# Optimization experiments

Hardware: AMD Instinct MI355X
Metric: run time of the kernel (lower is better)

Reference implementation:

```python
import jax, jax.numpy as jnp
import numpy as np

B, C, H, W = 1, 256, 512, 512
DS = 4
HD, WD = H // DS, W // DS
N_NOISE = 32
N_CLUSTERS = 8


def setup_inputs() -> dict:
    key = jax.random.key(0)
    k1, k2, k3, k4, k5 = jax.random.split(key, 5)
    x = jax.random.normal(k1, (B, C, H, W), dtype=jnp.float32)
    # deterministic 'HDBSCAN' labels over the B*C=256 channel-tokens:
    # first 224 channels in 8 clusters of 28, last 32 channels are noise (-1)
    n_clustered = C - N_NOISE
    labels_np = np.concatenate([
        np.arange(n_clustered) % N_CLUSTERS,
        -np.ones(N_NOISE, dtype=np.int64),
    ]).astype(np.int32)
    labels = jnp.asarray(labels_np)
    noise_idx = jnp.arange(n_clustered, C, dtype=jnp.int32)  # channels with label -1
    # grouped 1x1 conv (groups=C, 3 outputs per channel): per-output scalar weight+bias
    w_qkv = jax.random.normal(k2, (3 * C,), dtype=jnp.float32) * 0.02
    b_qkv = jax.random.normal(k3, (3 * C,), dtype=jnp.float32) * 0.02
    # depthwise ConvTranspose2d(kernel=stride=DS, groups=C): per-channel DSxDS kernel
    w_up = jax.random.normal(k4, (C, DS, DS), dtype=jnp.float32) * 0.25
    b_up = jax.random.normal(k5, (C,), dtype=jnp.float32) * 0.02
    return {"x": x, "labels": labels, "noise_idx": noise_idx,
            "w_qkv": w_qkv, "b_qkv": b_qkv, "w_up": w_up, "b_up": b_up}


def _l2norm(a):
    n = jnp.linalg.norm(a, axis=-1, keepdims=True)
    return a / jnp.maximum(n, 1e-12)


def reference(x, labels, noise_idx, w_qkv, b_qkv, w_up, b_up):
    # --- MaxPool2d(DS, DS) ---  (B=1)
    xd = x.reshape(C, HD, DS, WD, DS).max(axis=(2, 4))          # (C, HD, WD)
    xdf = xd.reshape(C, HD * WD)                                 # (C, hw)
    # --- grouped 1x1 qkv conv: out channel o = x[o//3]*w[o]+b[o]; then chunk(3)
    #     reproduces the torch code exactly, incl. its interleaved channel layout ---
    qkv = jnp.repeat(xdf, 3, axis=0) * w_qkv[:, None] + b_qkv[:, None]  # (3C, hw)
    q, k, v = qkv[:C], qkv[C:2 * C], qkv[2 * C:]
    # --- per-cluster attention as a single masked softmax over C tokens ---
    valid = labels != -1
    same = (labels[:, None] == labels[None, :]) & valid[:, None] & valid[None, :]
    scores = q @ k.T                                             # (C, C), no scaling (as in source)
    scores = jnp.where(same, scores, jnp.finfo(scores.dtype).min)
    attn = jax.nn.softmax(scores, axis=-1)
    attn = jnp.where(valid[:, None], attn, 0.0)                  # noise rows -> 0 output
    out_ds = attn @ v                                            # (C, hw)
    # --- depthwise ConvTranspose2d, stride==kernel -> non-overlapping blocks ---
    out_sp = out_ds.reshape(C, HD, WD)
    up = jnp.einsum('chw,cab->chawb', out_sp, w_up).reshape(C, H, W)
    up = (up + b_up[:, None, None])[None]                        # (1, C, H, W)
    # --- noise features & cosine similarity ---
    nf = x.reshape(B, C, H * W)[:, noise_idx, :]                 # (B, n_noise, HW)
    cf = up.reshape(B, C, H * W)                                 # (B, C, HW)
    sim = jnp.einsum('bch,bnh->bcn', _l2norm(cf), _l2norm(nf)).mean(axis=-1)  # (B, C)
    similar = sim.reshape(B, C, 1, 1)
    out = up + (1.0 - similar) * x
    return out, nf.reshape(B, N_NOISE, H, W)
```

## Files before the change

### kernel.cpp

```cpp
#include <hip/hip_runtime.h>
#include <math.h>

#define C_ 256
#define H_ 512
#define W_ 512
#define HW_ (H_*W_)
#define HD_ 128
#define WD_ 128
#define P_ (HD_*WD_)
#define NN_ 32
#define GR_ 86
#define NSL_ 128

#define XD_OFF     0ull
#define SDS_OFF    4194304ull
#define GT_OFF     8388608ull
#define GPART_OFF  8650752ull
#define DSTP_OFF   8650752ull
#define S_OFF      9641984ull
#define SPART_OFF  9642240ull
#define NSQP_OFF   9650432ull
#define GSUMP_OFF  9651456ull
#define BETA_OFF   9651968ull
#define M_OFF      9652224ull
#define SCALE_OFF  9674752ull

typedef float nfloat4 __attribute__((ext_vector_type(4)));

__device__ __forceinline__ void nt_store4(float4 v, float* p) {
    nfloat4 nv;
    nv.x = v.x; nv.y = v.y; nv.z = v.z; nv.w = v.w;
    __builtin_nontemporal_store(nv, (nfloat4*)p);
}

__device__ __forceinline__ float4 nt_load4(const float* p) {
    nfloat4 nv = __builtin_nontemporal_load((const nfloat4*)p);
    float4 v;
    v.x = nv.x; v.y = nv.y; v.z = nv.z; v.w = nv.w;
    return v;
}

__device__ __forceinline__ float wsum64(float v) {
#pragma unroll
    for (int off = 32; off > 0; off >>= 1) v += __shfl_down(v, off, 64);
    return v;
}

__global__ void __launch_bounds__(256) k_pre(
        const float* __restrict__ x, const int* __restrict__ nidx,
        float* __restrict__ xd, float* __restrict__ outnf,
        float* __restrict__ Spart, float* __restrict__ nsqp) {
    int b = blockIdx.x;
    int c = b >> 5, seg = b & 31;
    int t = threadIdx.x;
    __shared__ int sn;
    if (t == 0) {
        int nn = -1;
        for (int n = 0; n < NN_; n++)
            if (nidx[n] == c) nn = n;
        sn = nn;
    }
    __syncthreads();
    int n = sn;
    int wd = t & 127;
    int hl = t >> 7;
    float ssum = 0.f, ss = 0.f;
    const float* xc = x + (size_t)c * HW_;
    float* nfc = outnf + (size_t)(n < 0 ? 0 : n) * HW_;
#pragma unroll
    for (int q = 0; q < 2; q++) {
        int hd = 4 * seg + hl + 2 * q;
        const float4* xr = (const float4*)(xc + (size_t)(4 * hd) * W_) + wd;
        float4 r0 = xr[0], r1 = xr[128], r2 = xr[256], r3 = xr[384];
        if (n >= 0) {
            float* nr = nfc + (size_t)(4 * hd) * W_ + 4 * wd;
            nt_store4(r0, nr);
            nt_store4(r1, nr + 512);
            nt_store4(r2, nr + 1024);
            nt_store4(r3, nr + 1536);
            ss += r0.x*r0.x + r0.y*r0.y + r0.z*r0.z + r0.w*r0.w
                + r1.x*r1.x + r1.y*r1.y + r1.z*r1.z + r1.w*r1.w
                + r2.x*r2.x + r2.y*r2.y + r2.z*r2.z + r2.w*r2.w
                + r3.x*r3.x + r3.y*r3.y + r3.z*r3.z + r3.w*r3.w;
        }
        float m0 = fmaxf(fmaxf(r0.x, r0.y), fmaxf(r0.z, r0.w));
        float m1 = fmaxf(fmaxf(r1.x, r1.y), fmaxf(r1.z, r1.w));
        float m2 = fmaxf(fmaxf(r2.x, r2.y), fmaxf(r2.z, r2.w));
        float m3 = fmaxf(fmaxf(r3.x, r3.y), fmaxf(r3.z, r3.w));
        float m = fmaxf(fmaxf(m0, m1), fmaxf(m2, m3));
        xd[(size_t)c * P_ + (size_t)hd * WD_ + wd] = m;
        ssum += m;
    }
    __shared__ float red[4];
    float tt = wsum64(ssum);
    int wid = t >> 6, ln = t & 63;
    if (ln == 0) red[wid] = tt;
    __syncthreads();
    if (t == 0) Spart[c * 32 + seg] = red[0] + red[1] + red[2] + red[3];
    if (n >= 0) {
        __syncthreads();
        float t2 = wsum64(ss);
        if (ln == 0) red[wid] = t2;
        __syncthreads();
        if (t == 0) nsqp[n * 32 + seg] = red[0] + red[1] + red[2] + red[3];
    }
}

__global__ void __launch_bounds__(256) k_mid(
        const float* __restrict__ x, const int* __restrict__ nidx,
        const float* __restrict__ nsqp, const float* __restrict__ Spart,
        const float* __restrict__ xd,
        float* __restrict__ gt, float* __restrict__ gsump,
        float* __restrict__ gpart, float* __restrict__ S) {
    __shared__ float smem[2 * 32 * 132];
    int bid = blockIdx.x;
    int t = threadIdx.x;
    if (bid < 512) {
        float* inv_ = smem;
        int* ncs = (int*)(smem + 32);
        float* red = smem + 64;
        float4* comb = (float4*)(smem + 128);
        if (t < NN_) {
            const float* np = nsqp + t * 32;
            float s = 0.f;
#pragma unroll
            for (int k = 0; k < 32; k++) s += np[k];
            inv_[t] = (1.f / 32.f) / fmaxf(sqrtf(s), 1e-12f);
            ncs[t] = nidx[t];
        }
        __syncthreads();
        int h = bid >> 2, a = bid & 3;
        int w = t & 127, half = t >> 7;
        size_t rowoff = (size_t)(4 * h + a) * W_ + 4 * w;
        float4 acc = make_float4(0.f, 0.f, 0.f, 0.f);
#pragma unroll
        for (int k = 0; k < 16; k++) {
            int n = half * 16 + k;
            float4 v = *(const float4*)(x + (size_t)ncs[n] * HW_ + rowoff);
            float iv = inv_[n];
            acc.x += v.x * iv; acc.y += v.y * iv;
            acc.z += v.z * iv; acc.w += v.w * iv;
        }
        comb[t] = acc;
        float gs = acc.x + acc.y + acc.z + acc.w;
        float tt = wsum64(gs);
        int wid = t >> 6, ln = t & 63;
        if (ln == 0) red[wid] = tt;
        __syncthreads();
        if (t == 0) gsump[bid] = red[0] + red[1] + red[2] + red[3];
        if (t < 128) {
            float4 u = comb[t], v2 = comb[t + 128];
            float g0 = u.x + v2.x, g1 = u.y + v2.y, g2 = u.z + v2.z, g3 = u.w + v2.w;
            size_t pbase = (size_t)(a * 4) * P_ + h * WD_ + w;
            gt[pbase] = g0;
            gt[pbase + P_] = g1;
            gt[pbase + 2 * P_] = g2;
            gt[pbase + 3 * P_] = g3;
        }
    } else if (bid < 512 + NSL_) {
        int sl = bid - 512;
        float (*As)[132] = (float(*)[132])smem;
        float (*Bs)[132] = (float(*)[132])(smem + 32 * 132);
        int tx = t & 15, ty = t >> 4;
        int p0 = sl * 128;
        float acc[8][8];
#pragma unroll
        for (int i = 0; i < 8; i++)
#pragma unroll
            for (int j = 0; j < 8; j++) acc[i][j] = 0.f;
        for (int ch = 0; ch < 4; ch++) {
            int pb = p0 + ch * 32;
            __syncthreads();
#pragma unroll
            for (int kk = 0; kk < 16; kk++) {
                int lin = kk * 256 + t;
                int row = lin >> 5;
                int pp = lin & 31;
                float av = 0.f, bv = 0.f;
                if (row < GR_) {
                    av = xd[(size_t)row * P_ + pb + pp];
                    bv = xd[(size_t)(85 + row) * P_ + pb + pp];
                }
                As[pp][row] = av;
                Bs[pp][row] = bv;
            }
            __syncthreads();
            for (int pp = 0; pp < 32; pp++) {
                float4 fa0 = *(const float4*)&As[pp][8 * tx];
                float4 fa1 = *(const float4*)&As[pp][8 * tx + 4];
                float4 fb0 = *(const float4*)&Bs[pp][8 * ty];
                float4 fb1 = *(const float4*)&Bs[pp][8 * ty + 4];
                float fa[8] = {fa0.x, fa0.y, fa0.z, fa0.w, fa1.x, fa1.y, fa1.z, fa1.w};
                float fb[8] = {fb0.x, fb0.y, fb0.z, fb0.w, fb1.x, fb1.y, fb1.z, fb1.w};
#pragma unroll
                for (int ii = 0; ii < 8; ii++)
#pragma unroll
                    for (int jj = 0; jj < 8; jj++) acc[ii][jj] += fa[ii] * fb[jj];
            }
        }
        float* gp = gpart + (size_t)sl * 7744;
#pragma unroll
        for (int ii = 0; ii < 8; ii++) {
            int ga = 8 * tx + ii;
            if (ga < GR_) {
#pragma unroll
                for (int jj = 0; jj < 8; jj++) {
                    int gb = 8 * ty + jj;
                    if (gb < GR_) gp[ga * 88 + gb] = acc[ii][jj];
                }
            }
        }
    } else {
        if (t < C_) {
            const float* sp = Spart + t * 32;
            float s = 0.f;
#pragma unroll
            for (int k = 0; k < 32; k++) s += sp[k];
            S[t] = s;
        }
    }
}

__global__ void __launch_bounds__(256) k_attn(
        const int* __restrict__ labels, const float* __restrict__ wqkv,
        const float* __restrict__ bqkv, const float* __restrict__ gpart,
        const float* __restrict__ S, float* __restrict__ M,
        float* __restrict__ beta) {
    int i = blockIdx.x, j = threadIdx.x;
    __shared__ float grow[GR_];
    __shared__ float Mloc[GR_];
    __shared__ float red[4];
    __shared__ float bc;
    int li = labels[i];
    if (li < 0) {
        if (j < GR_) M[i * 88 + j] = 0.f;
        if (j == 0) beta[i] = 0.f;
        return;
    }
    int a = i / 3;
    if (j < GR_) {
        Mloc[j] = 0.f;
        const float* gp = gpart + (size_t)a * 88 + j;
        float s = 0.f;
#pragma unroll 8
        for (int sl = 0; sl < NSL_; sl++) s += gp[(size_t)sl * 7744];
        grow[j] = s;
    }
    __syncthreads();
    float wq = wqkv[i], bq = bqkv[i];
    int kidx = 256 + j;
    int bk = kidx / 3;
    float wk = wqkv[kidx], bkb = bqkv[kidx];
    int lj = labels[j];
    bool same = (lj == li);
    float score = -3.0e38f;
    if (same)
        score = wq * wk * grow[bk - 85] + wq * bkb * S[a] + bq * wk * S[bk] +
                16384.f * bq * bkb;
    int wid = j >> 6, ln = j & 63;
    float m = score;
#pragma unroll
    for (int off = 32; off > 0; off >>= 1) m = fmaxf(m, __shfl_down(m, off, 64));
    if (ln == 0) red[wid] = m;
    __syncthreads();
    if (j == 0) bc = fmaxf(fmaxf(red[0], red[1]), fmaxf(red[2], red[3]));
    __syncthreads();
    float mx = bc;
    float e = same ? expf(score - mx) : 0.f;
    __syncthreads();
    float t = wsum64(e);
    if (ln == 0) red[wid] = t;
    __syncthreads();
    if (j == 0) bc = red[0] + red[1] + red[2] + red[3];
    __syncthreads();
    float attn = e / bc;
    int vidx = 512 + j;
    int vr = vidx / 3 - 170;
    float wv = wqkv[vidx], bv = bqkv[vidx];
    __syncthreads();
    float bp = wsum64(attn * bv);
    if (ln == 0) red[wid] = bp;
    __syncthreads();
    if (j == 0) beta[i] = red[0] + red[1] + red[2] + red[3];
    atomicAdd(&Mloc[vr], attn * wv);
    __syncthreads();
    if (j < GR_) M[i * 88 + j] = Mloc[j];
}

__global__ void __launch_bounds__(256) k_outds(
        const float* __restrict__ xd, const float* __restrict__ gt,
        const float* __restrict__ M, const float* __restrict__ beta,
        float* __restrict__ sds, float* __restrict__ dstp) {
    __shared__ float Mt[16][88];
    __shared__ float bt[16];
    __shared__ float sdsL[16][258];
    __shared__ float gtsL[16][258];
    int t = threadIdx.x;
    int p0 = blockIdx.x * 256;
    int i0 = blockIdx.y * 16;
    for (int idx = t; idx < 16 * 88; idx += 256)
        Mt[idx / 88][idx % 88] = M[(size_t)(i0 + idx / 88) * 88 + (idx % 88)];
    if (t < 16) bt[t] = beta[i0 + t];
#pragma unroll 4
    for (int ab = 0; ab < 16; ab++)
        gtsL[ab][t] = gt[(size_t)ab * P_ + p0 + t];
    __syncthreads();
    float acc[16];
#pragma unroll
    for (int ii = 0; ii < 16; ii++) acc[ii] = bt[ii];
    const float* xb = xd + (size_t)170 * P_ + p0 + t;
    for (int r = 0; r < 84; r += 4) {
        float x0 = xb[(size_t)r * P_];
        float x1 = xb[(size_t)(r + 1) * P_];
        float x2 = xb[(size_t)(r + 2) * P_];
        float x3 = xb[(size_t)(r + 3) * P_];
#pragma unroll
        for (int ii = 0; ii < 16; ii++) {
            float4 mv = *(const float4*)&Mt[ii][r];
            acc[ii] += mv.x * x0 + mv.y * x1 + mv.z * x2 + mv.w * x3;
        }
    }
    {
        float x0 = xb[(size_t)84 * P_];
        float x1 = xb[(size_t)85 * P_];
#pragma unroll
        for (int ii = 0; ii < 16; ii++)
            acc[ii] += Mt[ii][84] * x0 + Mt[ii][85] * x1;
    }
#pragma unroll
    for (int ii = 0; ii < 16; ii++) {
        sds[(size_t)(i0 + ii) * P_ + p0 + t] = acc[ii];
        sdsL[ii][t] = acc[ii];
    }
    __syncthreads();
    int ch = t & 15, ab = t >> 4;
    bool do1 = (t < 16), do2 = (t >= 16 && t < 32);
    float D = 0.f, sx = 0.f;
    for (int k = 0; k < 256; k++) {
        float sv = sdsL[ch][k];
        float gv = gtsL[ab][k];
        D += sv * gv;
        if (do1) sx += sv;
        if (do2) sx += sv * sv;
    }
    size_t base = ((size_t)(i0 + ch) * 64 + blockIdx.x) * 18;
    dstp[base + ab] = D;
    if (do1) dstp[base + 16] = sx;
    if (do2) dstp[base + 17] = sx;
}

__global__ void __launch_bounds__(64) k_sim(
        const float* __restrict__ dstp, const float* __restrict__ gsump,
        const float* __restrict__ wup, const float* __restrict__ bup,
        float* __restrict__ scale) {
    int c = blockIdx.x, t = threadIdx.x;
    const float* dp = dstp + ((size_t)c * 64 + t) * 18;
    float vals[19];
#pragma unroll
    for (int q = 0; q < 18; q++) vals[q] = dp[q];
    float gsl = 0.f;
#pragma unroll
    for (int k = 0; k < 8; k++) gsl += gsump[t + 64 * k];
    vals[18] = gsl;
#pragma unroll
    for (int q = 0; q < 19; q++) vals[q] = wsum64(vals[q]);
    if (t == 0) {
        float gs = vals[18];
        float wsm = 0.f, wsq = 0.f, dd = 0.f;
#pragma unroll
        for (int ab = 0; ab < 16; ab++) {
            float w = wup[c * 16 + ab];
            wsm += w;
            wsq += w * w;
            dd += w * vals[ab];
        }
        float s1 = vals[16], s2 = vals[17];
        float b = bup[c];
        float dot = dd + b * gs;
        float n2 = wsq * s2 + 2.f * b * wsm * s1 + (float)HW_ * b * b;
        float nrm = sqrtf(fmaxf(n2, 0.f));
        scale[c] = 1.f - dot / fmaxf(nrm, 1e-12f);
    }
}

__global__ void __launch_bounds__(256) k_final(
        const float* __restrict__ x, const float* __restrict__ sds,
        const float* __restrict__ wup, const float* __restrict__ bup,
        const float* __restrict__ scale, float* __restrict__ out) {
    int bid = blockIdx.x;
    int c = bid >> 7, hd = bid & 127;
    int t = threadIdx.x;
    int wq = t & 127, ysub = t >> 7;
    float sv = sds[(size_t)c * P_ + (size_t)hd * WD_ + wq];
    float b = bup[c];
    float sc = scale[c];
    float4 wu0 = *(const float4*)(wup + c * 16 + ysub * 4);
    float4 wu1 = *(const float4*)(wup + c * 16 + (ysub + 2) * 4);
    size_t xoff = ((size_t)c * H_ + 4 * hd + ysub) * W_ + 4 * wq;
    float4 x0 = nt_load4(x + xoff);
    float4 x1 = nt_load4(x + xoff + 2 * W_);
    float4 o0, o1;
    o0.x = sv * wu0.x + b + sc * x0.x;
    o0.y = sv * wu0.y + b + sc * x0.y;
    o0.z = sv * wu0.z + b + sc * x0.z;
    o0.w = sv * wu0.w + b + sc * x0.w;
    o1.x = sv * wu1.x + b + sc * x1.x;
    o1.y = sv * wu1.y + b + sc * x1.y;
    o1.z = sv * wu1.z + b + sc * x1.z;
    o1.w = sv * wu1.w + b + sc * x1.w;
    nt_store4(o0, out + xoff);
    nt_store4(o1, out + xoff + 2 * W_);
}

extern "C" void kernel_launch(void* const* d_in, const int* in_sizes, int n_in,
                              void* d_out, int out_size, void* d_ws, size_t ws_size,
                              hipStream_t stream) {
    const float* x = (const float*)d_in[0];
    const int* labels = (const int*)d_in[1];
    const int* nidx = (const int*)d_in[2];
    const float* wqkv = (const float*)d_in[3];
    const float* bqkv = (const float*)d_in[4];
    const float* wup = (const float*)d_in[5];
    const float* bup = (const float*)d_in[6];
    float* out = (float*)d_out;
    float* ws = (float*)d_ws;

    float* xd = ws + XD_OFF;
    float* sds = ws + SDS_OFF;
    float* gt = ws + GT_OFF;
    float* gpart = ws + GPART_OFF;
    float* dstp = ws + DSTP_OFF;
    float* S = ws + S_OFF;
    float* Spart = ws + SPART_OFF;
    float* nsqp = ws + NSQP_OFF;
    float* gsump = ws + GSUMP_OFF;
    float* beta = ws + BETA_OFF;
    float* M = ws + M_OFF;
    float* scale = ws + SCALE_OFF;
    float* outnf = out + (size_t)C_ * HW_;

    k_pre<<<C_ * 32, 256, 0, stream>>>(x, nidx, xd, outnf, Spart, nsqp);
    k_mid<<<512 + NSL_ + 1, 256, 0, stream>>>(x, nidx, nsqp, Spart, xd, gt, gsump, gpart, S);
    k_attn<<<256, 256, 0, stream>>>(labels, wqkv, bqkv, gpart, S, M, beta);
    k_outds<<<dim3(64, 16), 256, 0, stream>>>(xd, gt, M, beta, sds, dstp);
    k_sim<<<256, 64, 0, stream>>>(dstp, gsump, wup, bup, scale);
    k_final<<<32768, 256, 0, stream>>>(x, sds, wup, bup, scale, out);
}
```

Measured before the change: 214.6 us.

## Fuse all stages into one cooperative persistent kernel with grid syncs

Replaces the six separate kernel launches with a single cooperative kernel of 512 persistent blocks. Each stage loops over its work units and the stages are separated by grid.sync(), so inter-kernel launch gaps and tail drains go away. The original launch sequence is kept as a fallback if the cooperative launch fails. The gram GEMM tile also shrinks from 8x8 to 6x6 per thread with scalar LDS reads. The cost is fewer resident blocks for the bandwidth-bound pre and final stages, plus the overhead of grid-wide barriers.

```diff
diff --git a/kernel.cpp b/kernel.cpp
--- a/kernel.cpp
+++ b/kernel.cpp
@@ -1,5 +1,8 @@
 #include <hip/hip_runtime.h>
+#include <hip/hip_cooperative_groups.h>
 #include <math.h>
+
+namespace cg = cooperative_groups;
 
 #define C_ 256
 #define H_ 512
@@ -11,6 +14,7 @@
 #define NN_ 32
 #define GR_ 86
 #define NSL_ 128
+#define NBLK 512
 
 #define XD_OFF     0ull
 #define SDS_OFF    4194304ull
@@ -25,6 +29,8 @@
 #define M_OFF      9652224ull
 #define SCALE_OFF  9674752ull
 
+#define SMEM_FLOATS 9680
+
 typedef float nfloat4 __attribute__((ext_vector_type(4)));
 
 __device__ __forceinline__ void nt_store4(float4 v, float* p) {
@@ -46,22 +52,22 @@
     return v;
 }
 
-__global__ void __launch_bounds__(256) k_pre(
-        const float* __restrict__ x, const int* __restrict__ nidx,
+__device__ __forceinline__ void pre_unit(
+        int u, const float* __restrict__ x, const int* __restrict__ nidx,
         float* __restrict__ xd, float* __restrict__ outnf,
-        float* __restrict__ Spart, float* __restrict__ nsqp) {
-    int b = blockIdx.x;
-    int c = b >> 5, seg = b & 31;
+        float* __restrict__ Spart, float* __restrict__ nsqp, float* smem) {
+    int c = u >> 5, seg = u & 31;
     int t = threadIdx.x;
-    __shared__ int sn;
+    float* red = smem;
+    int* snp = (int*)(smem + 4);
     if (t == 0) {
         int nn = -1;
         for (int n = 0; n < NN_; n++)
             if (nidx[n] == c) nn = n;
-        sn = nn;
-    }
-    __syncthreads();
-    int n = sn;
+        *snp = nn;
+    }
+    __syncthreads();
+    int n = *snp;
     int wd = t & 127;
     int hl = t >> 7;
     float ssum = 0.f, ss = 0.f;
@@ -91,7 +97,6 @@
         xd[(size_t)c * P_ + (size_t)hd * WD_ + wd] = m;
         ssum += m;
     }
-    __shared__ float red[4];
     float tt = wsum64(ssum);
     int wid = t >> 6, ln = t & 63;
     if (ln == 0) red[wid] = tt;
@@ -104,18 +109,17 @@
         __syncthreads();
         if (t == 0) nsqp[n * 32 + seg] = red[0] + red[1] + red[2] + red[3];
     }
-}
-
-__global__ void __launch_bounds__(256) k_mid(
-        const float* __restrict__ x, const int* __restrict__ nidx,
+    __syncthreads();
+}
+
+__device__ __forceinline__ void mid_unit(
+        int u, const float* __restrict__ x, const int* __restrict__ nidx,
         const float* __restrict__ nsqp, const float* __restrict__ Spart,
         const float* __restrict__ xd,
         float* __restrict__ gt, float* __restrict__ gsump,
-        float* __restrict__ gpart, float* __restrict__ S) {
-    __shared__ float smem[2 * 32 * 132];
-    int bid = blockIdx.x;
+        float* __restrict__ gpart, float* __restrict__ S, float* smem) {
     int t = threadIdx.x;
-    if (bid < 512) {
+    if (u < 512) {
         float* inv_ = smem;
         int* ncs = (int*)(smem + 32);
         float* red = smem + 64;
@@ -129,7 +133,7 @@
             ncs[t] = nidx[t];
         }
         __syncthreads();
-        int h = bid >> 2, a = bid & 3;
+        int h = u >> 2, a = u & 3;
         int w = t & 127, half = t >> 7;
         size_t rowoff = (size_t)(4 * h + a) * W_ + 4 * w;
         float4 acc = make_float4(0.f, 0.f, 0.f, 0.f);
@@ -147,27 +151,27 @@
         int wid = t >> 6, ln = t & 63;
         if (ln == 0) red[wid] = tt;
         __syncthreads();
-        if (t == 0) gsump[bid] = red[0] + red[1] + red[2] + red[3];
+        if (t == 0) gsump[u] = red[0] + red[1] + red[2] + red[3];
         if (t < 128) {
-            float4 u = comb[t], v2 = comb[t + 128];
-            float g0 = u.x + v2.x, g1 = u.y + v2.y, g2 = u.z + v2.z, g3 = u.w + v2.w;
+            float4 uu = comb[t], v2 = comb[t + 128];
             size_t pbase = (size_t)(a * 4) * P_ + h * WD_ + w;
-            gt[pbase] = g0;
-            gt[pbase + P_] = g1;
-            gt[pbase + 2 * P_] = g2;
-            gt[pbase + 3 * P_] = g3;
-        }
-    } else if (bid < 512 + NSL_) {
-        int sl = bid - 512;
+            gt[pbase] = uu.x + v2.x;
+            gt[pbase + P_] = uu.y + v2.y;
+            gt[pbase + 2 * P_] = uu.z + v2.z;
+            gt[pbase + 3 * P_] = uu.w + v2.w;
+        }
+        __syncthreads();
+    } else if (u < 512 + NSL_) {
+        int sl = u - 512;
         float (*As)[132] = (float(*)[132])smem;
         float (*Bs)[132] = (float(*)[132])(smem + 32 * 132);
         int tx = t & 15, ty = t >> 4;
         int p0 = sl * 128;
-        float acc[8][8];
-#pragma unroll
-        for (int i = 0; i < 8; i++)
-#pragma unroll
-            for (int j = 0; j < 8; j++) acc[i][j] = 0.f;
+        float acc[6][6];
+#pragma unroll
+        for (int i = 0; i < 6; i++)
+#pragma unroll
+            for (int j = 0; j < 6; j++) acc[i][j] = 0.f;
         for (int ch = 0; ch < 4; ch++) {
             int pb = p0 + ch * 32;
             __syncthreads();
@@ -186,26 +190,26 @@
             }
             __syncthreads();
             for (int pp = 0; pp < 32; pp++) {
-                float4 fa0 = *(const float4*)&As[pp][8 * tx];
-                float4 fa1 = *(const float4*)&As[pp][8 * tx + 4];
-                float4 fb0 = *(const float4*)&Bs[pp][8 * ty];
-                float4 fb1 = *(const float4*)&Bs[pp][8 * ty + 4];
-                float fa[8] = {fa0.x, fa0.y, fa0.z, fa0.w, fa1.x, fa1.y, fa1.z, fa1.w};
-                float fb[8] = {fb0.x, fb0.y, fb0.z, fb0.w, fb1.x, fb1.y, fb1.z, fb1.w};
-#pragma unroll
-                for (int ii = 0; ii < 8; ii++)
-#pragma unroll
-                    for (int jj = 0; jj < 8; jj++) acc[ii][jj] += fa[ii] * fb[jj];
+                float fa[6], fb[6];
+#pragma unroll
+                for (int i = 0; i < 6; i++) fa[i] = As[pp][6 * tx + i];
+#pragma unroll
+                for (int j = 0; j < 6; j++) fb[j] = Bs[pp][6 * ty + j];
+#pragma unroll
+                for (int ii = 0; ii < 6; ii++)
+#pragma unroll
+                    for (int jj = 0; jj < 6; jj++) acc[ii][jj] += fa[ii] * fb[jj];
             }
         }
+        __syncthreads();
         float* gp = gpart + (size_t)sl * 7744;
 #pragma unroll
-        for (int ii = 0; ii < 8; ii++) {
-            int ga = 8 * tx + ii;
+        for (int ii = 0; ii < 6; ii++) {
+            int ga = 6 * tx + ii;
             if (ga < GR_) {
 #pragma unroll
-                for (int jj = 0; jj < 8; jj++) {
-                    int gb = 8 * ty + jj;
+                for (int jj = 0; jj < 6; jj++) {
+                    int gb = 6 * ty + jj;
                     if (gb < GR_) gp[ga * 88 + gb] = acc[ii][jj];
                 }
             }
@@ -218,19 +222,20 @@
             for (int k = 0; k < 32; k++) s += sp[k];
             S[t] = s;
         }
-    }
-}
-
-__global__ void __launch_bounds__(256) k_attn(
-        const int* __restrict__ labels, const float* __restrict__ wqkv,
+        __syncthreads();
+    }
+}
+
+__device__ __forceinline__ void attn_unit(
+        int i, const int* __restrict__ labels, const float* __restrict__ wqkv,
         const float* __restrict__ bqkv, const float* __restrict__ gpart,
         const float* __restrict__ S, float* __restrict__ M,
-        float* __restrict__ beta) {
-    int i = blockIdx.x, j = threadIdx.x;
-    __shared__ float grow[GR_];
-    __shared__ float Mloc[GR_];
-    __shared__ float red[4];
-    __shared__ float bc;
+        float* __restrict__ beta, float* smem) {
+    int j = threadIdx.x;
+    float* grow = smem;
+    float* Mloc = smem + 96;
+    float* red = smem + 192;
+    float* bcp = smem + 196;
     int li = labels[i];
     if (li < 0) {
         if (j < GR_) M[i * 88 + j] = 0.f;
@@ -263,17 +268,17 @@
     for (int off = 32; off > 0; off >>= 1) m = fmaxf(m, __shfl_down(m, off, 64));
     if (ln == 0) red[wid] = m;
     __syncthreads();
-    if (j == 0) bc = fmaxf(fmaxf(red[0], red[1]), fmaxf(red[2], red[3]));
-    __syncthreads();
-    float mx = bc;
+    if (j == 0) *bcp = fmaxf(fmaxf(red[0], red[1]), fmaxf(red[2], red[3]));
+    __syncthreads();
+    float mx = *bcp;
     float e = same ? expf(score - mx) : 0.f;
     __syncthreads();
     float t = wsum64(e);
     if (ln == 0) red[wid] = t;
     __syncthreads();
-    if (j == 0) bc = red[0] + red[1] + red[2] + red[3];
-    __syncthreads();
-    float attn = e / bc;
+    if (j == 0) *bcp = red[0] + red[1] + red[2] + red[3];
+    __syncthreads();
+    float attn = e / *bcp;
     int vidx = 512 + j;
     int vr = vidx / 3 - 170;
     float wv = wqkv[vidx], bv = bqkv[vidx];
@@ -287,17 +292,18 @@
     if (j < GR_) M[i * 88 + j] = Mloc[j];
 }
 
-__global__ void __launch_bounds__(256) k_outds(
-        const float* __restrict__ xd, const float* __restrict__ gt,
+__device__ __forceinline__ void outds_unit(
+        int px, int iy, const float* __restrict__ xd, const float* __restrict__ gt,
         const float* __restrict__ M, const float* __restrict__ beta,
-        float* __restrict__ sds, float* __restrict__ dstp) {
-    __shared__ float Mt[16][88];
-    __shared__ float bt[16];
-    __shared__ float sdsL[16][258];
-    __shared__ float gtsL[16][258];
+        float* __restrict__ sds, float* __restrict__ dstp, float* smem) {
+    float (*Mt)[88] = (float(*)[88])smem;
+    float* bt = smem + 1408;
+    float (*sdsL)[258] = (float(*)[258])(smem + 1424);
+    float (*gtsL)[258] = (float(*)[258])(smem + 5552);
     int t = threadIdx.x;
-    int p0 = blockIdx.x * 256;
-    int i0 = blockIdx.y * 16;
+    int p0 = px * 256;
+    int i0 = iy * 16;
+    __syncthreads();
     for (int idx = t; idx < 16 * 88; idx += 256)
         Mt[idx / 88][idx % 88] = M[(size_t)(i0 + idx / 88) * 88 + (idx % 88)];
     if (t < 16) bt[t] = beta[i0 + t];
@@ -343,17 +349,17 @@
         if (do1) sx += sv;
         if (do2) sx += sv * sv;
     }
-    size_t base = ((size_t)(i0 + ch) * 64 + blockIdx.x) * 18;
+    size_t base = ((size_t)(i0 + ch) * 64 + px) * 18;
     dstp[base + ab] = D;
     if (do1) dstp[base + 16] = sx;
     if (do2) dstp[base + 17] = sx;
 }
 
-__global__ void __launch_bounds__(64) k_sim(
-        const float* __restrict__ dstp, const float* __restrict__ gsump,
+__device__ __forceinline__ void sim_unit(
+        int c, const float* __restrict__ dstp, const float* __restrict__ gsump,
         const float* __restrict__ wup, const float* __restrict__ bup,
         float* __restrict__ scale) {
-    int c = blockIdx.x, t = threadIdx.x;
+    int t = threadIdx.x;
     const float* dp = dstp + ((size_t)c * 64 + t) * 18;
     float vals[19];
 #pragma unroll
@@ -383,12 +389,43 @@
     }
 }
 
-__global__ void __launch_bounds__(256) k_final(
-        const float* __restrict__ x, const float* __restrict__ sds,
+__device__ __forceinline__ void final_block(
+        int bid, const float* __restrict__ x, const float* __restrict__ sds,
         const float* __restrict__ wup, const float* __restrict__ bup,
         const float* __restrict__ scale, float* __restrict__ out) {
-    int bid = blockIdx.x;
-    int c = bid >> 7, hd = bid & 127;
+    int c = bid >> 1, hbase = (bid & 1) << 6;
+    int t = threadIdx.x;
+    int wq = t & 127, ysub = t >> 7;
+    float b = bup[c], sc = scale[c];
+    float4 wu0 = *(const float4*)(wup + c * 16 + ysub * 4);
+    float4 wu1 = *(const float4*)(wup + c * 16 + (ysub + 2) * 4);
+    const float* sdc = sds + (size_t)c * P_ + wq;
+#pragma unroll 4
+    for (int k = 0; k < 64; k++) {
+        int hd = hbase + k;
+        float sv = sdc[(size_t)hd * WD_];
+        size_t xoff = ((size_t)c * H_ + 4 * hd + ysub) * W_ + 4 * wq;
+        float4 x0 = nt_load4(x + xoff);
+        float4 x1 = nt_load4(x + xoff + 2 * W_);
+        float4 o0, o1;
+        o0.x = sv * wu0.x + b + sc * x0.x;
+        o0.y = sv * wu0.y + b + sc * x0.y;
+        o0.z = sv * wu0.z + b + sc * x0.z;
+        o0.w = sv * wu0.w + b + sc * x0.w;
+        o1.x = sv * wu1.x + b + sc * x1.x;
+        o1.y = sv * wu1.y + b + sc * x1.y;
+        o1.z = sv * wu1.z + b + sc * x1.z;
+        o1.w = sv * wu1.w + b + sc * x1.w;
+        nt_store4(o0, out + xoff);
+        nt_store4(o1, out + xoff + 2 * W_);
+    }
+}
+
+__device__ __forceinline__ void final_unit(
+        int u, const float* __restrict__ x, const float* __restrict__ sds,
+        const float* __restrict__ wup, const float* __restrict__ bup,
+        const float* __restrict__ scale, float* __restrict__ out) {
+    int c = u >> 7, hd = u & 127;
     int t = threadIdx.x;
     int wq = t & 127, ysub = t >> 7;
     float sv = sds[(size_t)c * P_ + (size_t)hd * WD_ + wq];
@@ -412,18 +449,15 @@
     nt_store4(o1, out + xoff + 2 * W_);
 }
 
-extern "C" void kernel_launch(void* const* d_in, const int* in_sizes, int n_in,
-                              void* d_out, int out_size, void* d_ws, size_t ws_size,
-                              hipStream_t stream) {
-    const float* x = (const float*)d_in[0];
-    const int* labels = (const int*)d_in[1];
-    const int* nidx = (const int*)d_in[2];
-    const float* wqkv = (const float*)d_in[3];
-    const float* bqkv = (const float*)d_in[4];
-    const float* wup = (const float*)d_in[5];
-    const float* bup = (const float*)d_in[6];
-    float* out = (float*)d_out;
-    float* ws = (float*)d_ws;
+__global__ void __launch_bounds__(256) k_all(
+        const float* __restrict__ x, const int* __restrict__ labels,
+        const int* __restrict__ nidx, const float* __restrict__ wqkv,
+        const float* __restrict__ bqkv, const float* __restrict__ wup,
+        const float* __restrict__ bup, float* __restrict__ out,
+        float* __restrict__ ws) {
+    cg::grid_group grid = cg::this_grid();
+    __shared__ float smem[SMEM_FLOATS];
+    int bid = blockIdx.x;
 
     float* xd = ws + XD_OFF;
     float* sds = ws + SDS_OFF;
@@ -439,10 +473,118 @@
     float* scale = ws + SCALE_OFF;
     float* outnf = out + (size_t)C_ * HW_;
 
-    k_pre<<<C_ * 32, 256, 0, stream>>>(x, nidx, xd, outnf, Spart, nsqp);
-    k_mid<<<512 + NSL_ + 1, 256, 0, stream>>>(x, nidx, nsqp, Spart, xd, gt, gsump, gpart, S);
-    k_attn<<<256, 256, 0, stream>>>(labels, wqkv, bqkv, gpart, S, M, beta);
-    k_outds<<<dim3(64, 16), 256, 0, stream>>>(xd, gt, M, beta, sds, dstp);
-    k_sim<<<256, 64, 0, stream>>>(dstp, gsump, wup, bup, scale);
-    k_final<<<32768, 256, 0, stream>>>(x, sds, wup, bup, scale, out);
-}
+#pragma unroll 1
+    for (int k = 0; k < 16; k++)
+        pre_unit(bid + (k << 9), x, nidx, xd, outnf, Spart, nsqp, smem);
+    grid.sync();
+
+#pragma unroll 1
+    for (int u = bid; u < 512 + NSL_ + 1; u += NBLK)
+        mid_unit(u, x, nidx, nsqp, Spart, xd, gt, gsump, gpart, S, smem);
+    grid.sync();
+
+    if (bid < 256)
+        attn_unit(bid, labels, wqkv, bqkv, gpart, S, M, beta, smem);
+    grid.sync();
+
+#pragma unroll 1
+    for (int u = bid; u < 1024; u += NBLK)
+        outds_unit(u & 63, u >> 6, xd, gt, M, beta, sds, dstp, smem);
+    grid.sync();
+
+    if (bid < 256 && threadIdx.x < 64)
+        sim_unit(bid, dstp, gsump, wup, bup, scale);
+    grid.sync();
+
+    final_block(bid, x, sds, wup, bup, scale, out);
+}
+
+__global__ void __launch_bounds__(256) g_pre(
+        const float* __restrict__ x, const int* __restrict__ nidx,
+        float* __restrict__ xd, float* __restrict__ outnf,
+        float* __restrict__ Spart, float* __restrict__ nsqp) {
+    __shared__ float sm[8];
+    pre_unit(blockIdx.x, x, nidx, xd, outnf, Spart, nsqp, sm);
+}
+
+__global__ void __launch_bounds__(256) g_mid(
+        const float* __restrict__ x, const int* __restrict__ nidx,
+        const float* __restrict__ nsqp, const float* __restrict__ Spart,
+        const float* __restrict__ xd, float* __restrict__ gt,
+        float* __restrict__ gsump, float* __restrict__ gpart,
+        float* __restrict__ S) {
+    __shared__ float sm[8448];
+    mid_unit(blockIdx.x, x, nidx, nsqp, Spart, xd, gt, gsump, gpart, S, sm);
+}
+
+__global__ void __launch_bounds__(256) g_attn(
+        const int* __restrict__ labels, const float* __restrict__ wqkv,
+        const float* __restrict__ bqkv, const float* __restrict__ gpart,
+        const float* __restrict__ S, float* __restrict__ M,
+        float* __restrict__ beta) {
+    __shared__ float sm[256];
+    attn_unit(blockIdx.x, labels, wqkv, bqkv, gpart, S, M, beta, sm);
+}
+
+__global__ void __launch_bounds__(256) g_outds(
+        const float* __restrict__ xd, const float* __restrict__ gt,
+        const float* __restrict__ M, const float* __restrict__ beta,
+        float* __restrict__ sds, float* __restrict__ dstp) {
+    __shared__ float sm[SMEM_FLOATS];
+    outds_unit(blockIdx.x & 63, blockIdx.x >> 6, xd, gt, M, beta, sds, dstp, sm);
+}
+
+__global__ void __launch_bounds__(64) g_sim(
+        const float* __restrict__ dstp, const float* __restrict__ gsump,
+        const float* __restrict__ wup, const float* __restrict__ bup,
+        float* __restrict__ scale) {
+    sim_unit(blockIdx.x, dstp, gsump, wup, bup, scale);
+}
+
+__global__ void __launch_bounds__(256) g_final(
+        const float* __restrict__ x, const float* __restrict__ sds,
+        const float* __restrict__ wup, const float* __restrict__ bup,
+        const float* __restrict__ scale, float* __restrict__ out) {
+    final_unit(blockIdx.x, x, sds, wup, bup, scale, out);
+}
+
+extern "C" void kernel_launch(void* const* d_in, const int* in_sizes, int n_in,
+                              void* d_out, int out_size, void* d_ws, size_t ws_size,
+                              hipStream_t stream) {
+    const float* x = (const float*)d_in[0];
+    const int* labels = (const int*)d_in[1];
+    const int* nidx = (const int*)d_in[2];
+    const float* wqkv = (const float*)d_in[3];
+    const float* bqkv = (const float*)d_in[4];
+    const float* wup = (const float*)d_in[5];
+    const float* bup = (const float*)d_in[6];
+    float* out = (float*)d_out;
+    float* ws = (float*)d_ws;
+
+    float* xd = ws + XD_OFF;
+    float* sds = ws + SDS_OFF;
+    float* gt = ws + GT_OFF;
+    float* gpart = ws + GPART_OFF;
+    float* dstp = ws + DSTP_OFF;
+    float* S = ws + S_OFF;
+    float* Spart = ws + SPART_OFF;
+    float* nsqp = ws + NSQP_OFF;
+    float* gsump = ws + GSUMP_OFF;
+    float* beta = ws + BETA_OFF;
+    float* M = ws + M_OFF;
+    float* scale = ws + SCALE_OFF;
+    float* outnf = out + (size_t)C_ * HW_;
+
+    void* args[] = {(void*)&x, (void*)&labels, (void*)&nidx, (void*)&wqkv,
+                    (void*)&bqkv, (void*)&wup, (void*)&bup, (void*)&out, (void*)&ws};
+    hipError_t err = hipLaunchCooperativeKernel((void*)k_all, dim3(NBLK), dim3(256),
+                                                args, 0, stream);
+    if (err != hipSuccess) {
+        g_pre<<<C_ * 32, 256, 0, stream>>>(x, nidx, xd, outnf, Spart, nsqp);
+        g_mid<<<512 + NSL_ + 1, 256, 0, stream>>>(x, nidx, nsqp, Spart, xd, gt, gsump, gpart, S);
+        g_attn<<<256, 256, 0, stream>>>(labels, wqkv, bqkv, gpart, S, M, beta);
+        g_outds<<<1024, 256, 0, stream>>>(xd, gt, M, beta, sds, dstp);
+        g_sim<<<256, 64, 0, stream>>>(dstp, gsump, wup, bup, scale);
+        g_final<<<32768, 256, 0, stream>>>(x, sds, wup, bup, scale, out);
+    }
+}
```

Result: slower. 528.4 us (+146.2%).
